# Kernel optimization log

Hardware: AMD Instinct MI355X
Metric: run time of the kernel (lower is better)

The kernel has to match this reference:

```python
import jax, jax.numpy as jnp
import numpy as np

NEG_SLOPE = 0.2
BN_EPS = 1e-5
NUM_GRAPHS = 500


def gat_conv(x, src, dst, W, att_src, att_dst, bias, num_nodes):
    # x: [N, Fin], W: [Fin, H*C], att_*: [H, C], bias: [H*C]
    H, C = att_src.shape
    xh = (x @ W).reshape(num_nodes, H, C)                      # [N,H,C]
    a_src = jnp.einsum('nhc,hc->nh', xh, att_src)              # [N,H]
    a_dst = jnp.einsum('nhc,hc->nh', xh, att_dst)              # [N,H]
    e = jax.nn.leaky_relu(a_src[src] + a_dst[dst], NEG_SLOPE)  # [E,H]
    m = jax.ops.segment_max(e, dst, num_segments=num_nodes)    # [N,H]
    m = jnp.where(jnp.isfinite(m), m, 0.0)
    ee = jnp.exp(e - m[dst])
    s = jax.ops.segment_sum(ee, dst, num_segments=num_nodes)   # [N,H]
    alpha = ee / (s[dst] + 1e-16)                              # [E,H]
    out = jax.ops.segment_sum(alpha[:, :, None] * xh[src], dst,
                              num_segments=num_nodes)          # [N,H,C]
    return out.reshape(num_nodes, H * C) + bias


def bn_eval(x, gamma, beta, rmean, rvar):
    return (x - rmean) * jax.lax.rsqrt(rvar + BN_EPS) * gamma + beta


def setup_inputs() -> dict:
    key = jax.random.key(0)
    ks = jax.random.split(key, 24)
    N, E, F_in, A = 50000, 1600000, 32, 16
    inp = {
        'x': jax.random.normal(ks[0], (N, F_in), jnp.float32),
        'edge_index': jax.random.randint(ks[1], (2, E), 0, N, jnp.int32),
        'batch': jnp.sort(jax.random.randint(ks[2], (N,), 0, NUM_GRAPHS, jnp.int32)),
        'W1': jax.random.normal(ks[3], (F_in, 64), jnp.float32) * 0.1,
        'att_src1': jax.random.normal(ks[4], (4, 16), jnp.float32) * 0.1,
        'att_dst1': jax.random.normal(ks[5], (4, 16), jnp.float32) * 0.1,
        'b1': jnp.zeros((64,), jnp.float32),
        'bn1_g': jnp.ones((64,), jnp.float32),
        'bn1_b': jnp.zeros((64,), jnp.float32),
        'bn1_rm': jax.random.normal(ks[6], (64,), jnp.float32) * 0.1,
        'bn1_rv': jax.random.uniform(ks[7], (64,), jnp.float32) + 0.5,
        'W2': jax.random.normal(ks[8], (64, 128), jnp.float32) * 0.1,
        'att_src2': jax.random.normal(ks[9], (4, 32), jnp.float32) * 0.1,
        'att_dst2': jax.random.normal(ks[10], (4, 32), jnp.float32) * 0.1,
        'b2': jnp.zeros((128,), jnp.float32),
        'bn2_g': jnp.ones((128,), jnp.float32),
        'bn2_b': jnp.zeros((128,), jnp.float32),
        'bn2_rm': jax.random.normal(ks[11], (128,), jnp.float32) * 0.1,
        'bn2_rv': jax.random.uniform(ks[12], (128,), jnp.float32) + 0.5,
        # attention pooling gate
        'gate_W': jax.random.normal(ks[13], (128, 1), jnp.float32) * 0.1,
        'gate_b': jnp.zeros((1,), jnp.float32),
        # heads
        'fc1_W': jax.random.normal(ks[14], (128, 32), jnp.float32) * 0.1,
        'fc1_b': jnp.zeros((32,), jnp.float32),
        'val_W': jax.random.normal(ks[15], (32, 1), jnp.float32) * 0.1,
        'val_b': jnp.zeros((1,), jnp.float32),
        'adv_W': jax.random.normal(ks[16], (32, A), jnp.float32) * 0.1,
        'adv_b': jnp.zeros((A,), jnp.float32),
    }
    return inp


def reference(x, edge_index, batch, W1, att_src1, att_dst1, b1,
              bn1_g, bn1_b, bn1_rm, bn1_rv,
              W2, att_src2, att_dst2, b2,
              bn2_g, bn2_b, bn2_rm, bn2_rv,
              gate_W, gate_b, fc1_W, fc1_b,
              val_W, val_b, adv_W, adv_b):
    N = x.shape[0]
    # GATConv default add_self_loops=True
    loop = jnp.arange(N, dtype=edge_index.dtype)
    src = jnp.concatenate([edge_index[0], loop])
    dst = jnp.concatenate([edge_index[1], loop])

    h = gat_conv(x, src, dst, W1, att_src1, att_dst1, b1, N)
    h = jax.nn.relu(bn_eval(h, bn1_g, bn1_b, bn1_rm, bn1_rv))
    h = gat_conv(h, src, dst, W2, att_src2, att_dst2, b2, N)
    h = jax.nn.relu(bn_eval(h, bn2_g, bn2_b, bn2_rm, bn2_rv))

    # AttentionalAggregation: softmax(gate) over nodes per graph, weighted sum
    gate = h @ gate_W + gate_b                                  # [N,1]
    gmax = jax.ops.segment_max(gate, batch, num_segments=NUM_GRAPHS)
    gmax = jnp.where(jnp.isfinite(gmax), gmax, 0.0)
    ge = jnp.exp(gate - gmax[batch])
    gs = jax.ops.segment_sum(ge, batch, num_segments=NUM_GRAPHS)
    w = ge / (gs[batch] + 1e-16)                                # [N,1]
    pooled = jax.ops.segment_sum(w * h, batch, num_segments=NUM_GRAPHS)  # [G,128]

    z = jax.nn.relu(pooled @ fc1_W + fc1_b)
    value = z @ val_W + val_b                                   # [G,1]
    adv = z @ adv_W + adv_b                                     # [G,A]
    return value + (adv - adv.mean(axis=1, keepdims=True))
```

## Files before the change

### kernel.cpp

```cpp
#include <hip/hip_runtime.h>
#include <hip/hip_fp16.h>
#include <math.h>

#define NEG_SLOPE 0.2f
#define BN_EPS_F 1e-5f
#define NUM_G 500
#define NBUK_MAX 128
#define CHUNK 4096

__device__ __forceinline__ float leaky(float x){ return x > 0.f ? x : NEG_SLOPE*x; }
__device__ __forceinline__ float bcast(float v, int k){
  return __int_as_float(__builtin_amdgcn_readlane(__float_as_int(v), k));
}

#define HB 256
#define BB 64
#define L1B 512
__global__ __launch_bounds__(256) void fused_hist_lin1_kernel(
    const int* __restrict__ edst, int E, int* __restrict__ bukcnt,
    int bshift, int nbuk,
    const int* __restrict__ batch, int* __restrict__ gcnt,
    const float* __restrict__ x, const float* __restrict__ W,
    const float* __restrict__ att_s, const float* __restrict__ att_d,
    __half* __restrict__ xh, float* __restrict__ a_src, float* __restrict__ a_dst, int N)
{
  __shared__ int lhist[NUM_G];
  int t = threadIdx.x;
  int bid = blockIdx.x;
  if (bid < HB) {
    if (t < NBUK_MAX) lhist[t] = 0;
    __syncthreads();
    int i = bid*256 + t, stride = HB*256;
    for (; i < E; i += stride) atomicAdd(&lhist[edst[i] >> bshift], 1);
    __syncthreads();
    if (t < nbuk && lhist[t]) atomicAdd(&bukcnt[t], lhist[t]);
  } else if (bid < HB + BB) {
    for (int i = t; i < NUM_G; i += 256) lhist[i] = 0;
    __syncthreads();
    int i = (bid-HB)*256 + t, stride = BB*256;
    for (; i < N; i += stride) atomicAdd(&lhist[batch[i]], 1);
    __syncthreads();
    for (int i = t; i < NUM_G; i += 256) if (lhist[i]) atomicAdd(&gcnt[i], lhist[i]);
  } else {
    int lane = t & 63;
    int wid  = ((bid - HB - BB)*256 + t) >> 6;
    int nw   = (L1B*256) >> 6;
    float w[32];
    #pragma unroll
    for (int k = 0; k < 32; ++k) w[k] = W[k*64 + lane];
    float asv = att_s[lane], adv = att_d[lane];
    for (int n = wid; n < N; n += nw) {
      float xv = (lane < 32) ? x[(size_t)n*32 + lane] : 0.f;
      float acc = 0.f;
      #pragma unroll
      for (int k = 0; k < 32; ++k) acc = fmaf(bcast(xv, k), w[k], acc);
      float sv = acc*asv, dv = acc*adv;
      #pragma unroll
      for (int m = 1; m < 16; m <<= 1) { sv += __shfl_xor(sv, m); dv += __shfl_xor(dv, m); }
      xh[(size_t)n*64 + lane] = __float2half(acc);
      if ((lane & 15) == 0) { a_src[n*4 + (lane>>4)] = sv; a_dst[n*4 + (lane>>4)] = dv; }
    }
  }
}

__global__ __launch_bounds__(1024) void exscan2_kernel(
    const int* __restrict__ in0, int* __restrict__ out0, int n0,
    const int* __restrict__ in1, int* __restrict__ out1, int n1)
{
  const int* in  = blockIdx.x ? in1  : in0;
  int*       out = blockIdx.x ? out1 : out0;
  int        n   = blockIdx.x ? n1   : n0;
  __shared__ int part[1024];
  int t = threadIdx.x;
  int per = (n + 1023) >> 10;
  int lo = t*per, hi = lo + per; if (lo > n) lo = n; if (hi > n) hi = n;
  int s = 0;
  for (int i = lo; i < hi; ++i) s += in[i];
  part[t] = s;
  __syncthreads();
  for (int ofs = 1; ofs < 1024; ofs <<= 1) {
    int v = (t >= ofs) ? part[t-ofs] : 0;
    __syncthreads();
    part[t] += v;
    __syncthreads();
  }
  int base = part[t] - s;
  for (int i = lo; i < hi; ++i) { out[i] = base; base += in[i]; }
  if (t == 1023) out[n] = part[1023];
}

__global__ __launch_bounds__(256) void binscat_kernel(
    const int* __restrict__ esrc, const int* __restrict__ edst, int E,
    const int* __restrict__ bukoff, int* __restrict__ bukcur,
    int2* __restrict__ pairs, int bshift, int nbuk)
{
  __shared__ int hist[NBUK_MAX];
  __shared__ int loffs[NBUK_MAX];
  __shared__ int gbase[NBUK_MAX];
  __shared__ int2 stage[CHUNK];
  int t = threadIdx.x;
  for (int c0 = blockIdx.x*CHUNK; c0 < E; c0 += gridDim.x*CHUNK) {
    int cnt = E - c0; if (cnt > CHUNK) cnt = CHUNK;
    if (t < NBUK_MAX) hist[t] = 0;
    __syncthreads();
    for (int i = t; i < cnt; i += 256)
      atomicAdd(&hist[edst[c0+i] >> bshift], 1);
    __syncthreads();
    int cb = (t < nbuk) ? hist[t] : 0;
    for (int ofs = 1; ofs < nbuk; ofs <<= 1) {
      int v = (t < nbuk && t >= ofs) ? hist[t-ofs] : 0;
      __syncthreads();
      if (t < nbuk) hist[t] += v;
      __syncthreads();
    }
    if (t < nbuk) {
      int lo = hist[t] - cb;
      loffs[t] = lo;
      int base = atomicAdd(&bukcur[t], cb);
      gbase[t] = bukoff[t] + base - lo;
    }
    __syncthreads();
    if (t < nbuk) hist[t] = 0;
    __syncthreads();
    for (int i = t; i < cnt; i += 256) {
      int s = esrc[c0+i], d = edst[c0+i];
      int b = d >> bshift;
      int r = atomicAdd(&hist[b], 1);
      stage[loffs[b] + r] = make_int2(s, d);
    }
    __syncthreads();
    for (int j = t; j < cnt; j += 256) {
      int2 p = stage[j];
      pairs[gbase[p.y >> bshift] + j] = p;
    }
    __syncthreads();
  }
}

__global__ __launch_bounds__(512) void bucket_csr_kernel(
    const int2* __restrict__ pairs, const int* __restrict__ bukoff,
    int* __restrict__ off, int* __restrict__ csr, int N, int E, int bshift)
{
  __shared__ int cnt[1024];
  __shared__ int cur[1024];
  __shared__ int part[512];
  int b = blockIdx.x, t = threadIdx.x;
  int base = b << bshift;
  int bnodes = 1 << bshift;
  int nlocal = N - base; if (nlocal > bnodes) nlocal = bnodes;
  int lo = bukoff[b], hi = bukoff[b+1];
  int gb = lo;
  for (int i = t; i < bnodes; i += 512) cnt[i] = 0;
  __syncthreads();
  for (int i = lo + t; i < hi; i += 512) atomicAdd(&cnt[pairs[i].y - base], 1);
  __syncthreads();
  int Wc = bnodes >> 9;
  int mys = 0;
  for (int j = 0; j < Wc; ++j) mys += cnt[t*Wc + j];
  part[t] = mys;
  __syncthreads();
  for (int ofs = 1; ofs < 512; ofs <<= 1) {
    int v = (t >= ofs) ? part[t-ofs] : 0;
    __syncthreads();
    part[t] += v;
    __syncthreads();
  }
  int ex = part[t] - mys;
  for (int j = 0; j < Wc; ++j) { int c = cnt[t*Wc + j]; cnt[t*Wc + j] = ex; ex += c; }
  __syncthreads();
  for (int i = t; i < nlocal; i += 512) off[base + i] = gb + cnt[i];
  if (b == 0 && t == 0) off[N] = E;
  for (int i = t; i < bnodes; i += 512) cur[i] = 0;
  __syncthreads();
  for (int i = lo + t; i < hi; i += 512) {
    int2 p = pairs[i];
    int l = p.y - base;
    int pos = gb + cnt[l] + atomicAdd(&cur[l], 1);
    csr[pos] = p.x;
  }
}

__global__ __launch_bounds__(256) void gat_agg1_kernel(
    const __half* __restrict__ xh, const float* __restrict__ a_src, const float* __restrict__ a_dst,
    const int* __restrict__ off, const int* __restrict__ csr,
    const float* __restrict__ bias, const float* __restrict__ bng, const float* __restrict__ bnb,
    const float* __restrict__ bnrm, const float* __restrict__ bnrv,
    float* __restrict__ hout, int N)
{
  int lane = threadIdx.x & 63;
  int wid  = (blockIdx.x * blockDim.x + threadIdx.x) >> 6;
  int nw   = (gridDim.x * blockDim.x) >> 6;
  int h = lane >> 4;
  float sc  = rsqrtf(bnrv[lane]+BN_EPS_F) * bng[lane];
  float ofc = bias[lane]*sc + bnb[lane] - bnrm[lane]*sc;
  for (int n = wid; n < N; n += nw) {
    int e = off[n], hi = off[n+1];
    float adh = a_dst[n*4+h];
    float es  = __expf(leaky(a_src[n*4+h] + adh));
    float acc = 0.f, ssum = 0.f;
    for (; e+7 < hi; e += 8) {
      int s0=csr[e],   s1=csr[e+1], s2=csr[e+2], s3=csr[e+3];
      int s4=csr[e+4], s5=csr[e+5], s6=csr[e+6], s7=csr[e+7];
      float a0=a_src[s0*4+h], a1=a_src[s1*4+h], a2=a_src[s2*4+h], a3=a_src[s3*4+h];
      float a4=a_src[s4*4+h], a5=a_src[s5*4+h], a6=a_src[s6*4+h], a7=a_src[s7*4+h];
      float v0=__half2float(xh[(size_t)s0*64+lane]);
      float v1=__half2float(xh[(size_t)s1*64+lane]);
      float v2=__half2float(xh[(size_t)s2*64+lane]);
      float v3=__half2float(xh[(size_t)s3*64+lane]);
      float v4=__half2float(xh[(size_t)s4*64+lane]);
      float v5=__half2float(xh[(size_t)s5*64+lane]);
      float v6=__half2float(xh[(size_t)s6*64+lane]);
      float v7=__half2float(xh[(size_t)s7*64+lane]);
      float w0=__expf(leaky(a0+adh)), w1=__expf(leaky(a1+adh));
      float w2=__expf(leaky(a2+adh)), w3=__expf(leaky(a3+adh));
      float w4=__expf(leaky(a4+adh)), w5=__expf(leaky(a5+adh));
      float w6=__expf(leaky(a6+adh)), w7=__expf(leaky(a7+adh));
      ssum += ((w0+w1)+(w2+w3)) + ((w4+w5)+(w6+w7));
      acc = fmaf(w0,v0,acc); acc = fmaf(w1,v1,acc);
      acc = fmaf(w2,v2,acc); acc = fmaf(w3,v3,acc);
      acc = fmaf(w4,v4,acc); acc = fmaf(w5,v5,acc);
      acc = fmaf(w6,v6,acc); acc = fmaf(w7,v7,acc);
    }
    for (; e < hi; ++e) {
      int s = csr[e];
      float a = a_src[s*4+h];
      float v = __half2float(xh[(size_t)s*64+lane]);
      float w = __expf(leaky(a+adh));
      ssum += w; acc = fmaf(w,v,acc);
    }
    float vs = __half2float(xh[(size_t)n*64+lane]);
    acc  = fmaf(es, vs, acc);
    ssum += es;
    float val = acc / (ssum + 1e-16f);
    hout[(size_t)n*64+lane] = fmaxf(fmaf(val, sc, ofc), 0.f);
  }
}

__global__ __launch_bounds__(256) void lin2_kernel(
    const float* __restrict__ hin, const float* __restrict__ W,
    const float* __restrict__ att_s, const float* __restrict__ att_d,
    __half* __restrict__ xh, float* __restrict__ a_src, float* __restrict__ a_dst, int N)
{
  int lane = threadIdx.x & 63;
  int wid  = (blockIdx.x * blockDim.x + threadIdx.x) >> 6;
  int nw   = (gridDim.x * blockDim.x) >> 6;
  float wa[64], wb[64];
  #pragma unroll
  for (int k = 0; k < 64; ++k) { wa[k] = W[k*128 + lane]; wb[k] = W[k*128 + 64 + lane]; }
  float asa = att_s[lane], ada = att_d[lane];
  float asb = att_s[64+lane], adb = att_d[64+lane];
  for (int n = wid; n < N; n += nw) {
    float hv = hin[(size_t)n*64 + lane];
    float a0 = 0.f, a1 = 0.f;
    #pragma unroll
    for (int k = 0; k < 64; ++k) {
      float h = bcast(hv, k);
      a0 = fmaf(h, wa[k], a0); a1 = fmaf(h, wb[k], a1);
    }
    float sva = a0*asa, dva = a0*ada, svb = a1*asb, dvb = a1*adb;
    #pragma unroll
    for (int m = 1; m < 32; m <<= 1) {
      sva += __shfl_xor(sva, m); dva += __shfl_xor(dva, m);
      svb += __shfl_xor(svb, m); dvb += __shfl_xor(dvb, m);
    }
    xh[(size_t)n*128 + lane] = __float2half(a0);
    xh[(size_t)n*128 + 64 + lane] = __float2half(a1);
    if ((lane & 31) == 0) {
      int hh = lane >> 5;
      a_src[n*4 + hh] = sva;     a_dst[n*4 + hh] = dva;
      a_src[n*4 + 2 + hh] = svb; a_dst[n*4 + 2 + hh] = dvb;
    }
  }
}

__global__ __launch_bounds__(256) void gat_agg2_kernel(
    const __half* __restrict__ xh, const float* __restrict__ a_src, const float* __restrict__ a_dst,
    const int* __restrict__ off, const int* __restrict__ csr,
    const float* __restrict__ bias, const float* __restrict__ bng, const float* __restrict__ bnb,
    const float* __restrict__ bnrm, const float* __restrict__ bnrv,
    const float* __restrict__ gateW, const float* __restrict__ gateB,
    float* __restrict__ hout, float* __restrict__ gate, int N)
{
  int lane = threadIdx.x & 63;
  int wid  = (blockIdx.x * blockDim.x + threadIdx.x) >> 6;
  int nw   = (gridDim.x * blockDim.x) >> 6;
  int c2 = 2*lane, h = lane >> 4;
  float sc0  = rsqrtf(bnrv[c2  ]+BN_EPS_F) * bng[c2  ];
  float of0  = bias[c2  ]*sc0 + bnb[c2  ] - bnrm[c2  ]*sc0;
  float sc1  = rsqrtf(bnrv[c2+1]+BN_EPS_F) * bng[c2+1];
  float of1  = bias[c2+1]*sc1 + bnb[c2+1] - bnrm[c2+1]*sc1;
  float gw0 = gateW[c2], gw1 = gateW[c2+1], gb = gateB[0];
  const __half2* xhv = (const __half2*)xh;
  for (int n = wid; n < N; n += nw) {
    int e = off[n], hi = off[n+1];
    float adh = a_dst[n*4+h];
    float es  = __expf(leaky(a_src[n*4+h] + adh));
    float accx = 0.f, accy = 0.f, ssum = 0.f;
    for (; e+7 < hi; e += 8) {
      int s0=csr[e],   s1=csr[e+1], s2=csr[e+2], s3=csr[e+3];
      int s4=csr[e+4], s5=csr[e+5], s6=csr[e+6], s7=csr[e+7];
      float a0=a_src[s0*4+h], a1=a_src[s1*4+h], a2=a_src[s2*4+h], a3=a_src[s3*4+h];
      float a4=a_src[s4*4+h], a5=a_src[s5*4+h], a6=a_src[s6*4+h], a7=a_src[s7*4+h];
      __half2 v0 = xhv[(size_t)s0*64 + lane];
      __half2 v1 = xhv[(size_t)s1*64 + lane];
      __half2 v2 = xhv[(size_t)s2*64 + lane];
      __half2 v3 = xhv[(size_t)s3*64 + lane];
      __half2 v4 = xhv[(size_t)s4*64 + lane];
      __half2 v5 = xhv[(size_t)s5*64 + lane];
      __half2 v6 = xhv[(size_t)s6*64 + lane];
      __half2 v7 = xhv[(size_t)s7*64 + lane];
      float w0=__expf(leaky(a0+adh)), w1=__expf(leaky(a1+adh));
      float w2=__expf(leaky(a2+adh)), w3=__expf(leaky(a3+adh));
      float w4=__expf(leaky(a4+adh)), w5=__expf(leaky(a5+adh));
      float w6=__expf(leaky(a6+adh)), w7=__expf(leaky(a7+adh));
      ssum += ((w0+w1)+(w2+w3)) + ((w4+w5)+(w6+w7));
      float2 f0=__half22float2(v0), f1=__half22float2(v1);
      float2 f2=__half22float2(v2), f3=__half22float2(v3);
      float2 f4=__half22float2(v4), f5=__half22float2(v5);
      float2 f6=__half22float2(v6), f7=__half22float2(v7);
      accx = fmaf(w0,f0.x,accx); accy = fmaf(w0,f0.y,accy);
      accx = fmaf(w1,f1.x,accx); accy = fmaf(w1,f1.y,accy);
      accx = fmaf(w2,f2.x,accx); accy = fmaf(w2,f2.y,accy);
      accx = fmaf(w3,f3.x,accx); accy = fmaf(w3,f3.y,accy);
      accx = fmaf(w4,f4.x,accx); accy = fmaf(w4,f4.y,accy);
      accx = fmaf(w5,f5.x,accx); accy = fmaf(w5,f5.y,accy);
      accx = fmaf(w6,f6.x,accx); accy = fmaf(w6,f6.y,accy);
      accx = fmaf(w7,f7.x,accx); accy = fmaf(w7,f7.y,accy);
    }
    for (; e < hi; ++e) {
      int s = csr[e];
      float a = a_src[s*4+h];
      __half2 v = xhv[(size_t)s*64 + lane];
      float w = __expf(leaky(a+adh));
      float2 f = __half22float2(v);
      ssum += w; accx = fmaf(w,f.x,accx); accy = fmaf(w,f.y,accy);
    }
    float2 fs = __half22float2(xhv[(size_t)n*64 + lane]);
    accx = fmaf(es, fs.x, accx); accy = fmaf(es, fs.y, accy);
    ssum += es;
    float inv = 1.f / (ssum + 1e-16f);
    float r0 = fmaxf(fmaf(accx*inv, sc0, of0), 0.f);
    float r1 = fmaxf(fmaf(accy*inv, sc1, of1), 0.f);
    *(float2*)(hout + (size_t)n*128 + c2) = make_float2(r0, r1);
    float gl = r0*gw0 + r1*gw1;
    #pragma unroll
    for (int m = 1; m < 64; m <<= 1) gl += __shfl_xor(gl, m);
    if (lane == 0) gate[n] = gl + gb;
  }
}

__global__ __launch_bounds__(128) void pool_kernel(
    const float* __restrict__ h2, const float* __restrict__ gate, const int* __restrict__ goff,
    const float* __restrict__ fc1W, const float* __restrict__ fc1b,
    const float* __restrict__ valW, const float* __restrict__ valb,
    const float* __restrict__ advW, const float* __restrict__ advb,
    float* __restrict__ out)
{
  int g = blockIdx.x, t = threadIdx.x;
  int lo = goff[g], hi = goff[g+1];
  __shared__ float red[2];
  __shared__ float pld[128];
  __shared__ float zs[32];
  __shared__ float sval;
  __shared__ float adv_s[16];

  float m = -3.4e38f;
  for (int n = lo+t; n < hi; n += 128) m = fmaxf(m, gate[n]);
  #pragma unroll
  for (int msk = 1; msk < 64; msk <<= 1) m = fmaxf(m, __shfl_xor(m, msk));
  if ((t & 63) == 0) red[t >> 6] = m;
  __syncthreads();
  m = fmaxf(red[0], red[1]);
  __syncthreads();
  float sl = 0.f;
  for (int n = lo+t; n < hi; n += 128) sl += __expf(gate[n]-m);
  #pragma unroll
  for (int msk = 1; msk < 64; msk <<= 1) sl += __shfl_xor(sl, msk);
  if ((t & 63) == 0) red[t >> 6] = sl;
  __syncthreads();
  float s = red[0] + red[1];
  float acc = 0.f;
  for (int n = lo; n < hi; ++n) {
    float w = __expf(gate[n]-m);
    acc += w * h2[(size_t)n*128 + t];
  }
  pld[t] = acc / (s + 1e-16f);
  __syncthreads();
  if (t < 32) {
    float z = fc1b[t];
    #pragma unroll 4
    for (int k = 0; k < 128; ++k) z += pld[k]*fc1W[k*32 + t];
    zs[t] = fmaxf(z, 0.f);
  }
  __syncthreads();
  if (t < 32) {
    float pv = zs[t]*valW[t];
    #pragma unroll
    for (int msk = 1; msk < 32; msk <<= 1) pv += __shfl_xor(pv, msk);
    if (t == 0) sval = pv + valb[0];
  }
  if (t < 16) {
    float a = advb[t];
    #pragma unroll
    for (int k = 0; k < 32; ++k) a += zs[k]*advW[k*16 + t];
    adv_s[t] = a;
  }
  __syncthreads();
  if (t < 16) {
    float amean = adv_s[t];
    #pragma unroll
    for (int msk = 1; msk < 16; msk <<= 1) amean += __shfl_xor(amean, msk);
    amean *= (1.f/16.f);
    out[g*16 + t] = sval + adv_s[t] - amean;
  }
}

extern "C" void kernel_launch(void* const* d_in, const int* in_sizes, int n_in,
                              void* d_out, int out_size, void* d_ws, size_t ws_size,
                              hipStream_t stream)
{
  const float* x     = (const float*)d_in[0];
  const int*   eidx  = (const int*)  d_in[1];
  const int*   batch = (const int*)  d_in[2];
  const float* W1    = (const float*)d_in[3];
  const float* as1w  = (const float*)d_in[4];
  const float* ad1w  = (const float*)d_in[5];
  const float* b1    = (const float*)d_in[6];
  const float* bn1g  = (const float*)d_in[7];
  const float* bn1b  = (const float*)d_in[8];
  const float* bn1rm = (const float*)d_in[9];
  const float* bn1rv = (const float*)d_in[10];
  const float* W2    = (const float*)d_in[11];
  const float* as2w  = (const float*)d_in[12];
  const float* ad2w  = (const float*)d_in[13];
  const float* b2    = (const float*)d_in[14];
  const float* bn2g  = (const float*)d_in[15];
  const float* bn2b  = (const float*)d_in[16];
  const float* bn2rm = (const float*)d_in[17];
  const float* bn2rv = (const float*)d_in[18];
  const float* gateW = (const float*)d_in[19];
  const float* gateB = (const float*)d_in[20];
  const float* fc1W  = (const float*)d_in[21];
  const float* fc1b  = (const float*)d_in[22];
  const float* valW  = (const float*)d_in[23];
  const float* valb  = (const float*)d_in[24];
  const float* advW  = (const float*)d_in[25];
  const float* advb  = (const float*)d_in[26];

  int N = in_sizes[0] / 32;
  int E = in_sizes[1] / 2;
  const int* esrc = eidx;
  const int* edst = eidx + E;

  int bshift = 9;
  while ((((N - 1) >> bshift) + 1) > NBUK_MAX) ++bshift;
  int nbuk = ((N - 1) >> bshift) + 1;

  float* ws = (float*)d_ws;
  size_t o = 0;
  __half* xh1h = (__half*)(ws + o); o += (size_t)N*32;
  __half* xh2h = (__half*)(ws + o); o += (size_t)N*64;
  float* as1 = ws + o; o += (size_t)N*4;
  float* ad1 = ws + o; o += (size_t)N*4;
  float* as2 = ws + o; o += (size_t)N*4;
  float* ad2 = ws + o; o += (size_t)N*4;
  float* h1  = ws + o; o += (size_t)N*64;
  float* h2  = ws + o; o += (size_t)N*128;
  float* gate = ws + o; o += (size_t)N;
  if (o & 1) ++o;
  int2* pairs = (int2*)(ws + o); o += (size_t)E*2;
  int* ib     = (int*)(ws + o);
  int* gcnt   = ib;
  int* bukcnt = ib + 512;
  int* bukcur = ib + 640;
  size_t zcnt = 768;
  int* off    = ib + zcnt;
  int* goff   = off + (N+1);
  int* bukoff = goff + (NUM_G+1);
  int* csr    = bukoff + (NBUK_MAX+1);

  hipMemsetAsync(gcnt, 0, zcnt*sizeof(int), stream);

  fused_hist_lin1_kernel<<<HB+BB+L1B, 256, 0, stream>>>(
      edst, E, bukcnt, bshift, nbuk, batch, gcnt,
      x, W1, as1w, ad1w, xh1h, as1, ad1, N);
  exscan2_kernel<<<2, 1024, 0, stream>>>(bukcnt, bukoff, nbuk, gcnt, goff, NUM_G);
  int nchunk = (E + CHUNK - 1) / CHUNK;
  binscat_kernel<<<nchunk, 256, 0, stream>>>(esrc, edst, E, bukoff, bukcur, pairs, bshift, nbuk);
  bucket_csr_kernel<<<nbuk, 512, 0, stream>>>(pairs, bukoff, off, csr, N, E, bshift);
  gat_agg1_kernel<<<2048, 256, 0, stream>>>(xh1h, as1, ad1, off, csr,
      b1, bn1g, bn1b, bn1rm, bn1rv, h1, N);
  lin2_kernel<<<1024, 256, 0, stream>>>(h1, W2, as2w, ad2w, xh2h, as2, ad2, N);
  gat_agg2_kernel<<<2048, 256, 0, stream>>>(xh2h, as2, ad2, off, csr,
      b2, bn2g, bn2b, bn2rm, bn2rv, gateW, gateB, h2, gate, N);
  pool_kernel<<<NUM_G, 128, 0, stream>>>(h2, gate, goff, fc1W, fc1b, valW, valb, advW, advb,
      (float*)d_out);
}
```

Before: 291.1 us.

## Split wavefront into four edge groups with vectorized feature gathers in GAT aggregation

```diff
diff --git a/kernel.cpp b/kernel.cpp
--- a/kernel.cpp
+++ b/kernel.cpp
@@ -190,49 +190,54 @@
   int lane = threadIdx.x & 63;
   int wid  = (blockIdx.x * blockDim.x + threadIdx.x) >> 6;
   int nw   = (gridDim.x * blockDim.x) >> 6;
-  int h = lane >> 4;
-  float sc  = rsqrtf(bnrv[lane]+BN_EPS_F) * bng[lane];
-  float ofc = bias[lane]*sc + bnb[lane] - bnrm[lane]*sc;
+  int g  = lane >> 4;
+  int li = lane & 15;
+  int c0 = li * 4;
+  int h  = li >> 2;
+  float sc[4], of[4];
+  #pragma unroll
+  for (int j = 0; j < 4; ++j) {
+    sc[j] = rsqrtf(bnrv[c0+j]+BN_EPS_F) * bng[c0+j];
+    of[j] = bias[c0+j]*sc[j] + bnb[c0+j] - bnrm[c0+j]*sc[j];
+  }
   for (int n = wid; n < N; n += nw) {
-    int e = off[n], hi = off[n+1];
+    int lo = off[n], hi = off[n+1];
     float adh = a_dst[n*4+h];
     float es  = __expf(leaky(a_src[n*4+h] + adh));
-    float acc = 0.f, ssum = 0.f;
-    for (; e+7 < hi; e += 8) {
-      int s0=csr[e],   s1=csr[e+1], s2=csr[e+2], s3=csr[e+3];
-      int s4=csr[e+4], s5=csr[e+5], s6=csr[e+6], s7=csr[e+7];
-      float a0=a_src[s0*4+h], a1=a_src[s1*4+h], a2=a_src[s2*4+h], a3=a_src[s3*4+h];
-      float a4=a_src[s4*4+h], a5=a_src[s5*4+h], a6=a_src[s6*4+h], a7=a_src[s7*4+h];
-      float v0=__half2float(xh[(size_t)s0*64+lane]);
-      float v1=__half2float(xh[(size_t)s1*64+lane]);
-      float v2=__half2float(xh[(size_t)s2*64+lane]);
-      float v3=__half2float(xh[(size_t)s3*64+lane]);
-      float v4=__half2float(xh[(size_t)s4*64+lane]);
-      float v5=__half2float(xh[(size_t)s5*64+lane]);
-      float v6=__half2float(xh[(size_t)s6*64+lane]);
-      float v7=__half2float(xh[(size_t)s7*64+lane]);
-      float w0=__expf(leaky(a0+adh)), w1=__expf(leaky(a1+adh));
-      float w2=__expf(leaky(a2+adh)), w3=__expf(leaky(a3+adh));
-      float w4=__expf(leaky(a4+adh)), w5=__expf(leaky(a5+adh));
-      float w6=__expf(leaky(a6+adh)), w7=__expf(leaky(a7+adh));
-      ssum += ((w0+w1)+(w2+w3)) + ((w4+w5)+(w6+w7));
-      acc = fmaf(w0,v0,acc); acc = fmaf(w1,v1,acc);
-      acc = fmaf(w2,v2,acc); acc = fmaf(w3,v3,acc);
-      acc = fmaf(w4,v4,acc); acc = fmaf(w5,v5,acc);
-      acc = fmaf(w6,v6,acc); acc = fmaf(w7,v7,acc);
-    }
-    for (; e < hi; ++e) {
-      int s = csr[e];
+    float acc0=0.f, acc1=0.f, acc2=0.f, acc3=0.f, ssum=0.f;
+    for (int e = lo; e < hi; e += 4) {
+      int ee = e + g; bool ok = ee < hi;
+      int s = csr[ok ? ee : lo];
       float a = a_src[s*4+h];
-      float v = __half2float(xh[(size_t)s*64+lane]);
-      float w = __expf(leaky(a+adh));
-      ssum += w; acc = fmaf(w,v,acc);
-    }
-    float vs = __half2float(xh[(size_t)n*64+lane]);
-    acc  = fmaf(es, vs, acc);
+      int2 rv = *(const int2*)(xh + (size_t)s*64 + c0);
+      float w = ok ? __expf(leaky(a+adh)) : 0.f;
+      ssum += w;
+      float2 f0 = __half22float2(*(__half2*)&rv.x);
+      float2 f1 = __half22float2(*(__half2*)&rv.y);
+      acc0 = fmaf(w, f0.x, acc0); acc1 = fmaf(w, f0.y, acc1);
+      acc2 = fmaf(w, f1.x, acc2); acc3 = fmaf(w, f1.y, acc3);
+    }
+    #pragma unroll
+    for (int m = 16; m < 64; m <<= 1) {
+      acc0 += __shfl_xor(acc0, m); acc1 += __shfl_xor(acc1, m);
+      acc2 += __shfl_xor(acc2, m); acc3 += __shfl_xor(acc3, m);
+      ssum += __shfl_xor(ssum, m);
+    }
+    int2 rv = *(const int2*)(xh + (size_t)n*64 + c0);
+    float2 f0 = __half22float2(*(__half2*)&rv.x);
+    float2 f1 = __half22float2(*(__half2*)&rv.y);
+    acc0 = fmaf(es, f0.x, acc0); acc1 = fmaf(es, f0.y, acc1);
+    acc2 = fmaf(es, f1.x, acc2); acc3 = fmaf(es, f1.y, acc3);
     ssum += es;
-    float val = acc / (ssum + 1e-16f);
-    hout[(size_t)n*64+lane] = fmaxf(fmaf(val, sc, ofc), 0.f);
+    float inv = 1.f / (ssum + 1e-16f);
+    if (g == 0) {
+      float4 r;
+      r.x = fmaxf(fmaf(acc0*inv, sc[0], of[0]), 0.f);
+      r.y = fmaxf(fmaf(acc1*inv, sc[1], of[1]), 0.f);
+      r.z = fmaxf(fmaf(acc2*inv, sc[2], of[2]), 0.f);
+      r.w = fmaxf(fmaf(acc3*inv, sc[3], of[3]), 0.f);
+      *(float4*)(hout + (size_t)n*64 + c0) = r;
+    }
   }
 }
 
@@ -284,67 +289,77 @@
   int lane = threadIdx.x & 63;
   int wid  = (blockIdx.x * blockDim.x + threadIdx.x) >> 6;
   int nw   = (gridDim.x * blockDim.x) >> 6;
-  int c2 = 2*lane, h = lane >> 4;
-  float sc0  = rsqrtf(bnrv[c2  ]+BN_EPS_F) * bng[c2  ];
-  float of0  = bias[c2  ]*sc0 + bnb[c2  ] - bnrm[c2  ]*sc0;
-  float sc1  = rsqrtf(bnrv[c2+1]+BN_EPS_F) * bng[c2+1];
-  float of1  = bias[c2+1]*sc1 + bnb[c2+1] - bnrm[c2+1]*sc1;
-  float gw0 = gateW[c2], gw1 = gateW[c2+1], gb = gateB[0];
-  const __half2* xhv = (const __half2*)xh;
+  int g  = lane >> 4;
+  int li = lane & 15;
+  int c0 = li * 8;
+  int h  = li >> 2;
+  float sc[8], of[8], gw[8];
+  #pragma unroll
+  for (int j = 0; j < 8; ++j) {
+    sc[j] = rsqrtf(bnrv[c0+j]+BN_EPS_F) * bng[c0+j];
+    of[j] = bias[c0+j]*sc[j] + bnb[c0+j] - bnrm[c0+j]*sc[j];
+    gw[j] = gateW[c0+j];
+  }
+  float gb = gateB[0];
   for (int n = wid; n < N; n += nw) {
-    int e = off[n], hi = off[n+1];
+    int lo = off[n], hi = off[n+1];
     float adh = a_dst[n*4+h];
     float es  = __expf(leaky(a_src[n*4+h] + adh));
-    float accx = 0.f, accy = 0.f, ssum = 0.f;
-    for (; e+7 < hi; e += 8) {
-      int s0=csr[e],   s1=csr[e+1], s2=csr[e+2], s3=csr[e+3];
-      int s4=csr[e+4], s5=csr[e+5], s6=csr[e+6], s7=csr[e+7];
-      float a0=a_src[s0*4+h], a1=a_src[s1*4+h], a2=a_src[s2*4+h], a3=a_src[s3*4+h];
-      float a4=a_src[s4*4+h], a5=a_src[s5*4+h], a6=a_src[s6*4+h], a7=a_src[s7*4+h];
-      __half2 v0 = xhv[(size_t)s0*64 + lane];
-      __half2 v1 = xhv[(size_t)s1*64 + lane];
-      __half2 v2 = xhv[(size_t)s2*64 + lane];
-      __half2 v3 = xhv[(size_t)s3*64 + lane];
-      __half2 v4 = xhv[(size_t)s4*64 + lane];
-      __half2 v5 = xhv[(size_t)s5*64 + lane];
-      __half2 v6 = xhv[(size_t)s6*64 + lane];
-      __half2 v7 = xhv[(size_t)s7*64 + lane];
-      float w0=__expf(leaky(a0+adh)), w1=__expf(leaky(a1+adh));
-      float w2=__expf(leaky(a2+adh)), w3=__expf(leaky(a3+adh));
-      float w4=__expf(leaky(a4+adh)), w5=__expf(leaky(a5+adh));
-      float w6=__expf(leaky(a6+adh)), w7=__expf(leaky(a7+adh));
-      ssum += ((w0+w1)+(w2+w3)) + ((w4+w5)+(w6+w7));
-      float2 f0=__half22float2(v0), f1=__half22float2(v1);
-      float2 f2=__half22float2(v2), f3=__half22float2(v3);
-      float2 f4=__half22float2(v4), f5=__half22float2(v5);
-      float2 f6=__half22float2(v6), f7=__half22float2(v7);
-      accx = fmaf(w0,f0.x,accx); accy = fmaf(w0,f0.y,accy);
-      accx = fmaf(w1,f1.x,accx); accy = fmaf(w1,f1.y,accy);
-      accx = fmaf(w2,f2.x,accx); accy = fmaf(w2,f2.y,accy);
-      accx = fmaf(w3,f3.x,accx); accy = fmaf(w3,f3.y,accy);
-      accx = fmaf(w4,f4.x,accx); accy = fmaf(w4,f4.y,accy);
-      accx = fmaf(w5,f5.x,accx); accy = fmaf(w5,f5.y,accy);
-      accx = fmaf(w6,f6.x,accx); accy = fmaf(w6,f6.y,accy);
-      accx = fmaf(w7,f7.x,accx); accy = fmaf(w7,f7.y,accy);
-    }
-    for (; e < hi; ++e) {
-      int s = csr[e];
+    float acc0=0.f, acc1=0.f, acc2=0.f, acc3=0.f;
+    float acc4=0.f, acc5=0.f, acc6=0.f, acc7=0.f, ssum=0.f;
+    for (int e = lo; e < hi; e += 4) {
+      int ee = e + g; bool ok = ee < hi;
+      int s = csr[ok ? ee : lo];
       float a = a_src[s*4+h];
-      __half2 v = xhv[(size_t)s*64 + lane];
-      float w = __expf(leaky(a+adh));
-      float2 f = __half22float2(v);
-      ssum += w; accx = fmaf(w,f.x,accx); accy = fmaf(w,f.y,accy);
-    }
-    float2 fs = __half22float2(xhv[(size_t)n*64 + lane]);
-    accx = fmaf(es, fs.x, accx); accy = fmaf(es, fs.y, accy);
+      int4 rv = *(const int4*)(xh + (size_t)s*128 + c0);
+      float w = ok ? __expf(leaky(a+adh)) : 0.f;
+      ssum += w;
+      float2 f0 = __half22float2(*(__half2*)&rv.x);
+      float2 f1 = __half22float2(*(__half2*)&rv.y);
+      float2 f2 = __half22float2(*(__half2*)&rv.z);
+      float2 f3 = __half22float2(*(__half2*)&rv.w);
+      acc0 = fmaf(w, f0.x, acc0); acc1 = fmaf(w, f0.y, acc1);
+      acc2 = fmaf(w, f1.x, acc2); acc3 = fmaf(w, f1.y, acc3);
+      acc4 = fmaf(w, f2.x, acc4); acc5 = fmaf(w, f2.y, acc5);
+      acc6 = fmaf(w, f3.x, acc6); acc7 = fmaf(w, f3.y, acc7);
+    }
+    #pragma unroll
+    for (int m = 16; m < 64; m <<= 1) {
+      acc0 += __shfl_xor(acc0, m); acc1 += __shfl_xor(acc1, m);
+      acc2 += __shfl_xor(acc2, m); acc3 += __shfl_xor(acc3, m);
+      acc4 += __shfl_xor(acc4, m); acc5 += __shfl_xor(acc5, m);
+      acc6 += __shfl_xor(acc6, m); acc7 += __shfl_xor(acc7, m);
+      ssum += __shfl_xor(ssum, m);
+    }
+    int4 rv = *(const int4*)(xh + (size_t)n*128 + c0);
+    float2 f0 = __half22float2(*(__half2*)&rv.x);
+    float2 f1 = __half22float2(*(__half2*)&rv.y);
+    float2 f2 = __half22float2(*(__half2*)&rv.z);
+    float2 f3 = __half22float2(*(__half2*)&rv.w);
+    acc0 = fmaf(es, f0.x, acc0); acc1 = fmaf(es, f0.y, acc1);
+    acc2 = fmaf(es, f1.x, acc2); acc3 = fmaf(es, f1.y, acc3);
+    acc4 = fmaf(es, f2.x, acc4); acc5 = fmaf(es, f2.y, acc5);
+    acc6 = fmaf(es, f3.x, acc6); acc7 = fmaf(es, f3.y, acc7);
     ssum += es;
     float inv = 1.f / (ssum + 1e-16f);
-    float r0 = fmaxf(fmaf(accx*inv, sc0, of0), 0.f);
-    float r1 = fmaxf(fmaf(accy*inv, sc1, of1), 0.f);
-    *(float2*)(hout + (size_t)n*128 + c2) = make_float2(r0, r1);
-    float gl = r0*gw0 + r1*gw1;
-    #pragma unroll
-    for (int m = 1; m < 64; m <<= 1) gl += __shfl_xor(gl, m);
+    float r0 = fmaxf(fmaf(acc0*inv, sc[0], of[0]), 0.f);
+    float r1 = fmaxf(fmaf(acc1*inv, sc[1], of[1]), 0.f);
+    float r2 = fmaxf(fmaf(acc2*inv, sc[2], of[2]), 0.f);
+    float r3 = fmaxf(fmaf(acc3*inv, sc[3], of[3]), 0.f);
+    float r4 = fmaxf(fmaf(acc4*inv, sc[4], of[4]), 0.f);
+    float r5 = fmaxf(fmaf(acc5*inv, sc[5], of[5]), 0.f);
+    float r6 = fmaxf(fmaf(acc6*inv, sc[6], of[6]), 0.f);
+    float r7 = fmaxf(fmaf(acc7*inv, sc[7], of[7]), 0.f);
+    if (g == 0) {
+      float4 w0 = make_float4(r0, r1, r2, r3);
+      float4 w1 = make_float4(r4, r5, r6, r7);
+      *(float4*)(hout + (size_t)n*128 + c0)     = w0;
+      *(float4*)(hout + (size_t)n*128 + c0 + 4) = w1;
+    }
+    float gl = r0*gw[0] + r1*gw[1] + r2*gw[2] + r3*gw[3]
+             + r4*gw[4] + r5*gw[5] + r6*gw[6] + r7*gw[7];
+    #pragma unroll
+    for (int m = 1; m < 16; m <<= 1) gl += __shfl_xor(gl, m);
     if (lane == 0) gate[n] = gl + gb;
   }
 }
```

New measurement: 275.4 us. 1.06x faster.
